# Optimization experiments

Hardware: AMD Instinct MI355X
Metric: run time of the kernel (lower is better)

## Reference

```python
import jax, jax.numpy as jnp
import numpy as np

B, N, D, O, H, R = 32, 1024, 1024, 1024, 512, 64
TOPK = 4
MAX_GAIN = 0.1
SCALE = 1.0
LN_EPS = 1e-5


def _dct_basis(dim, num_bases):
    pos = np.arange(dim, dtype=np.float64)[None, :]
    modes = np.arange(num_bases, dtype=np.float64)[:, None]
    basis = np.cos(np.pi / dim * (pos + 0.5) * modes)
    basis[0] = basis[0] / np.sqrt(2.0)
    basis = basis * np.sqrt(2.0 / dim)
    return jnp.asarray(basis, jnp.float32)


def setup_inputs() -> dict:
    key = jax.random.key(0)
    ks = jax.random.split(key, 16)
    s = 0.02
    return {
        'x': jax.random.normal(ks[0], (B, N, D), jnp.float32),
        'context': jax.random.normal(ks[1], (B, H), jnp.float32),
        'input_basis': _dct_basis(D, R),                       # [R, D] (buffer)
        'output_basis': s * jax.random.normal(ks[2], (R, O), jnp.float32),
        'ln_gamma': jnp.ones((D,), jnp.float32),
        'ln_beta': jnp.zeros((D,), jnp.float32),
        'w1': s * jax.random.normal(ks[3], (D, H), jnp.float32),
        'b1': jnp.zeros((H,), jnp.float32),
        'w2': s * jax.random.normal(ks[4], (H, H), jnp.float32),
        'b2': jnp.zeros((H,), jnp.float32),
        'wg': s * jax.random.normal(ks[5], (H, R * R), jnp.float32),
        'bg': jnp.zeros((R * R,), jnp.float32),
        'wl': s * jax.random.normal(ks[6], (H, R * R), jnp.float32),
        'bl': jnp.zeros((R * R,), jnp.float32),
        'wm': s * jax.random.normal(ks[7], (2 * H, R), jnp.float32),
        'bm': 1.5 * jnp.ones((R,), jnp.float32),
        'wgain': s * jax.random.normal(ks[8], (2 * H, R), jnp.float32),
        'bgain': jnp.zeros((R,), jnp.float32),
        'wgate': s * jax.random.normal(ks[9], (2 * H, 1), jnp.float32),
        'bgate': -1.0 * jnp.ones((1,), jnp.float32),
        'wa': s * jax.random.normal(ks[10], (2 * H, 1), jnp.float32),
        'ba': -1.0 * jnp.ones((1,), jnp.float32),
        'wb': s * jax.random.normal(ks[11], (2 * H, 1), jnp.float32),
        'bb': jnp.zeros((1,), jnp.float32),
    }


def _detail_summary(x, topk):
    # x: [B, N, D] with token 0 = CLS; pick topk highest-variance patch tokens
    pt = x[:, 1:]                                   # [B, N-1, D]
    pm = jnp.mean(pt, axis=1, keepdims=True)
    scores = jnp.mean((pt - pm) ** 2, axis=-1)      # [B, N-1]
    _, idx = jax.lax.top_k(scores, topk)            # [B, k]
    gathered = jnp.take_along_axis(pt, idx[:, :, None], axis=1)  # [B, k, D]
    return jnp.mean(gathered, axis=1)               # [B, D]


def _skew(a):
    return 0.5 * (a - jnp.swapaxes(a, -1, -2))


def reference(x, context, input_basis, output_basis, ln_gamma, ln_beta,
              w1, b1, w2, b2, wg, bg, wl, bl, wm, bm,
              wgain, bgain, wgate, bgate, wa, ba, wb, bb):
    b = x.shape[0]
    r = input_basis.shape[0]

    detail = _detail_summary(x, TOPK)               # [B, D]
    mu = jnp.mean(detail, axis=-1, keepdims=True)
    var = jnp.var(detail, axis=-1, keepdims=True)
    h = (detail - mu) * jax.lax.rsqrt(var + LN_EPS) * ln_gamma + ln_beta
    h = jax.nn.gelu(h @ w1 + b1, approximate=False)
    local_context = h @ w2 + b2                     # [B, H]
    fused = jnp.concatenate([context, local_context], axis=-1)  # [B, 2H]

    global_skew = _skew((context @ wg + bg).reshape(b, r, r))
    local_skew = _skew((local_context @ wl + bl).reshape(b, r, r))
    mode_mask = jax.nn.sigmoid(fused @ wm + bm)     # [B, R]
    # diag(m) @ A @ diag(m) == m_i * A_ij * m_j
    mg = mode_mask[:, :, None] * global_skew * mode_mask[:, None, :]
    ml = mode_mask[:, :, None] * local_skew * mode_mask[:, None, :]
    comm = ml @ mg - mg @ ml                        # [B, R, R]

    alpha = SCALE * 0.5 * jax.nn.sigmoid(fused @ wa + ba)   # [B, 1]
    beta = SCALE * 0.25 * jnp.tanh(fused @ wb + bb)         # [B, 1]
    omega = alpha[:, :, None] * 0.5 * (mg + ml) + beta[:, :, None] * (comm / 12.0)

    q = jax.vmap(jax.scipy.linalg.expm)(omega)              # [B, R, R]
    gains = 1.0 + MAX_GAIN * jnp.tanh(fused @ wgain + bgain)  # [B, R]
    operator = q * gains[:, None, :]                        # q @ diag(gains)

    proj = jnp.einsum('bnd,rd->bnr', x, input_basis)        # [B, N, R]
    gate = SCALE * jax.nn.sigmoid(fused @ wgate + bgate)    # [B, 1]
    transformed = jnp.einsum('bnr,brk->bnk', proj, operator)
    delta = gate[:, None, :] * (transformed - proj)         # [B, N, R]
    out = jnp.einsum('bnr,ro->bno', delta, output_basis)    # [B, N, O]
    return out
```

## Files before the change

### kernel.cpp

```cpp
#include <hip/hip_runtime.h>
#include <math.h>

#define NB 32
#define NN 1024
#define ND 1024
#define NO 1024
#define NH 512
#define NR 64

#define OFF_PM     0u
#define OFF_PMSQ   32768u
#define OFF_ROWSQ  32800u
#define OFF_G      65568u
#define OFF_H0     98336u
#define OFF_H1     131104u
#define OFF_LOCAL  147488u
#define OFF_P1     163872u
#define OFF_P2     294944u
#define OFF_PG     360480u
#define OFF_PL     884768u
#define OFF_MFIN   1675424u
#define OFF_C      1806496u
#define OFF_PROJ   3903648u
#define OFF_BT     6000800u

#define AK(av,k) ((k&3)==0?av[(k)>>2].x:((k&3)==1?av[(k)>>2].y:((k&3)==2?av[(k)>>2].z:av[(k)>>2].w)))

__global__ __launch_bounds__(256) void kT_basis(const float* __restrict__ basis, float* __restrict__ basisT){
  __shared__ float s[64][65];
  int d0 = blockIdx.x*64;
  int tid = threadIdx.x;
  #pragma unroll
  for(int i=0;i<16;i++){
    int idx = i*256 + tid;
    int r = idx>>6, dl = idx&63;
    s[r][dl] = basis[(size_t)r*ND + d0 + dl];
  }
  __syncthreads();
  #pragma unroll
  for(int i=0;i<16;i++){
    int idx = i*256 + tid;
    int dl = idx>>6, r = idx&63;
    basisT[(size_t)(d0+dl)*64 + r] = s[r][dl];
  }
}

__global__ __launch_bounds__(256) void k0_colsum(const float* __restrict__ x, float* __restrict__ part,
    float* __restrict__ rowsq){
  __shared__ float red[4][64];
  int tid = threadIdx.x;
  int nseg = blockIdx.x, b = blockIdx.y;
  int d4 = tid*4;
  int lane = tid & 63, wv = tid >> 6;
  const float* xp = x + (size_t)b*NN*ND + d4;
  int nstart = nseg*64; if(nseg==0) nstart = 1;
  int nend = nseg*64 + 64;
  float sx=0.f, sy=0.f, sz=0.f, sw=0.f;
  #pragma unroll 4
  for(int n=nstart; n<nend; n++){
    float4 v = *(const float4*)&xp[(size_t)n*ND];
    sx+=v.x; sy+=v.y; sz+=v.z; sw+=v.w;
    float s = v.x*v.x + v.y*v.y + v.z*v.z + v.w*v.w;
    #pragma unroll
    for(int o=32;o>0;o>>=1) s += __shfl_down(s, o);
    if(lane==0) red[wv][n - nseg*64] = s;
  }
  *(float4*)&part[(size_t)(b*16+nseg)*1024 + d4] = make_float4(sx,sy,sz,sw);
  __syncthreads();
  if(tid < 64 && !(nseg==0 && tid==0)){
    rowsq[b*1024 + nseg*64 + tid] = red[0][tid]+red[1][tid]+red[2][tid]+red[3][tid];
  }
}

__global__ __launch_bounds__(256) void k1_pmreduce(const float* __restrict__ part, float* __restrict__ pm, float* __restrict__ pmsq){
  __shared__ float red[256];
  int b = blockIdx.x, tid = threadIdx.x;
  float acc = 0.f;
  #pragma unroll
  for(int i=0;i<4;i++){
    int d = i*256 + tid;
    float s = 0.f;
    #pragma unroll
    for(int ks=0;ks<16;ks++) s += part[(size_t)(b*16+ks)*1024 + d];
    float p = s * (1.0f/1023.0f);
    pm[b*1024+d] = p;
    acc += p*p;
  }
  red[tid] = acc; __syncthreads();
  for(int o=128;o>0;o>>=1){ if(tid<o) red[tid]+=red[tid+o]; __syncthreads(); }
  if(tid==0) pmsq[b] = red[0]*(1.0f/1024.0f);
}

__global__ __launch_bounds__(256) void k2_proj(const float* __restrict__ x, const float* __restrict__ bT,
    const float* __restrict__ pm, float* __restrict__ proj, float* __restrict__ projp,
    float* __restrict__ G, float* __restrict__ Gp){
  __shared__ __align__(16) float xs[64][68];
  __shared__ __align__(16) float bs[64][68];
  int tid = threadIdx.x;
  int row0 = blockIdx.x*64;
  int b = row0 >> 10;
  int kh = blockIdx.y;
  int kbase = kh*512;
  int lrow = tid>>4, lkv = tid&15;
  int rg = tid>>4, cg = tid&15;
  float acc[4][4];
  #pragma unroll
  for(int i_=0;i_<4;i_++){ acc[i_][0]=0.f; acc[i_][1]=0.f; acc[i_][2]=0.f; acc[i_][3]=0.f; }
  float gp[4]={0.f,0.f,0.f,0.f};
  int sw = ((lkv>>1)&3)<<2;
  for(int kc=0;kc<8;kc++){
    int k0 = kbase + kc*64;
    float4 p4 = *(const float4*)&pm[(size_t)b*ND + k0 + lkv*4];
    #pragma unroll
    for(int i=0;i<4;i++){
      int r = lrow + 16*i;
      float4 v = *(const float4*)&x[((size_t)(row0+r))*ND + k0 + lkv*4];
      int rs = r ^ sw;
      xs[lkv*4+0][rs]=v.x; xs[lkv*4+1][rs]=v.y; xs[lkv*4+2][rs]=v.z; xs[lkv*4+3][rs]=v.w;
      gp[i] += v.x*p4.x + v.y*p4.y + v.z*p4.z + v.w*p4.w;
    }
    #pragma unroll
    for(int i=0;i<4;i++){
      int idx = tid + 256*i;
      int kk = idx>>4, kv = idx&15;
      *(float4*)&bs[kk][kv*4] = *(const float4*)&bT[((size_t)(k0+kk))*64 + kv*4];
    }
    __syncthreads();
    #pragma unroll 8
    for(int kk=0;kk<64;kk++){
      float4 a = *(const float4*)&xs[kk][ (rg ^ ((kk>>3)&3)) << 2 ];
      float4 bb= *(const float4*)&bs[kk][cg*4];
      float ar[4]={a.x,a.y,a.z,a.w};
      float br[4]={bb.x,bb.y,bb.z,bb.w};
      #pragma unroll
      for(int i_=0;i_<4;i_++){
        #pragma unroll
        for(int j_=0;j_<4;j_++) acc[i_][j_] += ar[i_]*br[j_];
      }
    }
    __syncthreads();
  }
  float* dst = kh ? projp : proj;
  #pragma unroll
  for(int i_=0;i_<4;i_++){
    float4 v = make_float4(acc[i_][0],acc[i_][1],acc[i_][2],acc[i_][3]);
    *(float4*)&dst[((size_t)(row0 + rg*4 + i_))*NR + cg*4] = v;
  }
  __syncthreads();
  #pragma unroll
  for(int i=0;i<4;i++){ int r = lrow+16*i; bs[r][lkv]=gp[i]; }
  __syncthreads();
  if(tid<64){
    float g=0.f;
    #pragma unroll
    for(int c=0;c<16;c++) g += bs[tid][c];
    if(kh) Gp[row0+tid] = g; else G[row0+tid] = g;
  }
}

__global__ __launch_bounds__(256) void k2_red(float* __restrict__ proj, const float* __restrict__ projp){
  int id = blockIdx.x*256 + threadIdx.x;
  float4 a = *(const float4*)&proj[(size_t)id*4];
  float4 p = *(const float4*)&projp[(size_t)id*4];
  a.x+=p.x; a.y+=p.y; a.z+=p.z; a.w+=p.w;
  *(float4*)&proj[(size_t)id*4] = a;
}

__global__ __launch_bounds__(256) void k3_detail(const float* __restrict__ x, const float* __restrict__ rowsq,
    const float* __restrict__ G, const float* __restrict__ Gp, const float* __restrict__ pmsq,
    const float* __restrict__ gamma_, const float* __restrict__ beta_, float* __restrict__ h0){
  __shared__ float sc[1024];
  __shared__ float rv[256];
  __shared__ int ri[256];
  __shared__ int topi[4];
  __shared__ float mred[256];
  int b = blockIdx.x, tid = threadIdx.x;
  float ps = pmsq[b];
  const float invD = 1.0f/1024.0f;
  for(int n=tid;n<1024;n+=256)
    sc[n] = (n==0) ? -INFINITY : (rowsq[b*1024+n] - 2.0f*(G[b*1024+n]+Gp[b*1024+n]))*invD + ps;
  __syncthreads();
  for(int t=0;t<4;t++){
    float bv = -INFINITY; int bi = 0x7fffffff;
    for(int n=tid;n<1024;n+=256){
      float v = sc[n];
      if(v>bv || (v==bv && n<bi)){ bv=v; bi=n; }
    }
    rv[tid]=bv; ri[tid]=bi;
    __syncthreads();
    for(int o=128;o>0;o>>=1){
      if(tid<o){
        float v=rv[tid+o]; int ii=ri[tid+o];
        if(v>rv[tid] || (v==rv[tid] && ii<ri[tid])){ rv[tid]=v; ri[tid]=ii; }
      }
      __syncthreads();
    }
    if(tid==0){ topi[t]=ri[0]; sc[ri[0]] = -INFINITY; }
    __syncthreads();
  }
  int i0=topi[0], i1=topi[1], i2=topi[2], i3=topi[3];
  float dv[4]; float dsum=0.f;
  #pragma unroll
  for(int jj=0;jj<4;jj++){
    int d = tid + jj*256;
    float v = 0.25f*(x[((size_t)(b*NN+i0))*ND+d] + x[((size_t)(b*NN+i1))*ND+d]
                   + x[((size_t)(b*NN+i2))*ND+d] + x[((size_t)(b*NN+i3))*ND+d]);
    dv[jj]=v; dsum+=v;
  }
  mred[tid]=dsum; __syncthreads();
  for(int o=128;o>0;o>>=1){ if(tid<o) mred[tid]+=mred[tid+o]; __syncthreads(); }
  float mu = mred[0]*invD;
  __syncthreads();
  float vs=0.f;
  #pragma unroll
  for(int jj=0;jj<4;jj++){ float t2=dv[jj]-mu; vs+=t2*t2; }
  mred[tid]=vs; __syncthreads();
  for(int o=128;o>0;o>>=1){ if(tid<o) mred[tid]+=mred[tid+o]; __syncthreads(); }
  float var = mred[0]*invD;
  float rstd = rsqrtf(var + 1e-5f);
  #pragma unroll
  for(int jj=0;jj<4;jj++){
    int d = tid + jj*256;
    h0[b*1024+d] = (dv[jj]-mu)*rstd*gamma_[d] + beta_[d];
  }
}

__global__ __launch_bounds__(256) void gemm32_partial(const float* __restrict__ V, const float* __restrict__ W,
      float* __restrict__ part, int Kd, int Ncols){
  __shared__ __align__(16) float Vs[128][36];
  int col = blockIdx.x*256 + threadIdx.x;
  int k0 = blockIdx.y*128;
  for(int i=threadIdx.x; i<4096; i+=256){ int r=i>>7, k=i&127; Vs[k][r] = V[(size_t)r*Kd + k0 + k]; }
  __syncthreads();
  float acc[32];
  #pragma unroll
  for(int r=0;r<32;r++) acc[r]=0.f;
  #pragma unroll 4
  for(int k=0;k<128;k++){
    float wv = W[(size_t)(k0+k)*Ncols + col];
    #pragma unroll
    for(int r4=0;r4<8;r4++){
      float4 v = *(const float4*)&Vs[k][r4*4];
      acc[r4*4+0]+=v.x*wv; acc[r4*4+1]+=v.y*wv; acc[r4*4+2]+=v.z*wv; acc[r4*4+3]+=v.w*wv;
    }
  }
  #pragma unroll
  for(int r=0;r<32;r++) part[((size_t)(blockIdx.y*32 + r))*Ncols + col] = acc[r];
}

__global__ __launch_bounds__(256) void gemm32_gl(const float* __restrict__ ctx, const float* __restrict__ lcl,
    const float* __restrict__ wg, const float* __restrict__ wl,
    float* __restrict__ pg, float* __restrict__ pl){
  __shared__ __align__(16) float Vs[128][36];
  const float* V = blockIdx.z ? lcl : ctx;
  const float* W = blockIdx.z ? wl : wg;
  float* part    = blockIdx.z ? pl : pg;
  int col = blockIdx.x*256 + threadIdx.x;
  int k0 = blockIdx.y*128;
  for(int i=threadIdx.x; i<4096; i+=256){ int r=i>>7, k=i&127; Vs[k][r] = V[(size_t)r*512 + k0 + k]; }
  __syncthreads();
  float acc[32];
  #pragma unroll
  for(int r=0;r<32;r++) acc[r]=0.f;
  #pragma unroll 4
  for(int k=0;k<128;k++){
    float wv = W[(size_t)(k0+k)*4096 + col];
    #pragma unroll
    for(int r4=0;r4<8;r4++){
      float4 v = *(const float4*)&Vs[k][r4*4];
      acc[r4*4+0]+=v.x*wv; acc[r4*4+1]+=v.y*wv; acc[r4*4+2]+=v.z*wv; acc[r4*4+3]+=v.w*wv;
    }
  }
  #pragma unroll
  for(int r=0;r<32;r++) part[((size_t)(blockIdx.y*32 + r))*4096 + col] = acc[r];
}

__global__ __launch_bounds__(256) void k_red_gelu(const float* __restrict__ part, const float* __restrict__ b1, float* __restrict__ h1){
  int id = blockIdx.x*256 + threadIdx.x;
  int b_ = id >> 9, j = id & 511;
  float s = b1[j];
  #pragma unroll
  for(int ks=0;ks<8;ks++) s += part[(size_t)(ks*32+b_)*512 + j];
  h1[id] = 0.5f*s*(1.0f + erff(s*0.70710678118654752440f));
}
__global__ __launch_bounds__(256) void k_red_local(const float* __restrict__ part, const float* __restrict__ b2, float* __restrict__ lcl){
  int id = blockIdx.x*256 + threadIdx.x;
  int b_ = id >> 9, j = id & 511;
  float s = b2[j];
  #pragma unroll
  for(int ks=0;ks<4;ks++) s += part[(size_t)(ks*32+b_)*512 + j];
  lcl[id] = s;
}

__global__ __launch_bounds__(1024) void k7_fused(
    const float* __restrict__ pg, const float* __restrict__ pl,
    const float* __restrict__ bg, const float* __restrict__ bl,
    const float* __restrict__ context, const float* __restrict__ lcl,
    const float* __restrict__ wm, const float* __restrict__ bm,
    const float* __restrict__ wgain, const float* __restrict__ bgain,
    const float* __restrict__ wgate, const float* __restrict__ bgate,
    const float* __restrict__ wa, const float* __restrict__ ba,
    const float* __restrict__ wb, const float* __restrict__ bb,
    float* __restrict__ Mfin){
  __shared__ __align__(16) float B0s[64][68];
  __shared__ __align__(16) float B1s[64][68];
  __shared__ __align__(16) float B2s[64][68];
  __shared__ float fs[1024];
  __shared__ float redm[16][64];
  __shared__ float redg[16][64];
  __shared__ float wra[16], wrb[16], wrg[16];
  __shared__ float msks[64], gainss[64];
  __shared__ float colsum[64];
  __shared__ float sABG[3];
  __shared__ int ssh;
  int b = blockIdx.x, tid = threadIdx.x;

  int ig = tid>>5, jg = tid&31;
  int i0 = ig*2, j0 = jg*2;
  #pragma unroll
  for(int di=0;di<2;di++){
    #pragma unroll
    for(int dj=0;dj<2;dj++){
      int i=i0+di, jx=j0+dj, c=i*64+jx;
      float sg = bg[c], sl = bl[c];
      #pragma unroll
      for(int ks=0;ks<4;ks++){
        sg += pg[(size_t)(ks*32+b)*4096 + c];
        sl += pl[(size_t)(ks*32+b)*4096 + c];
      }
      B0s[i][jx] = sg; B1s[i][jx] = sl;
    }
  }
  fs[tid] = (tid < 512) ? context[b*512 + tid] : lcl[b*512 + tid - 512];
  __syncthreads();
  int j = tid & 63, kq = tid >> 6;
  {
    const float* wmp = wm    + (size_t)(kq*64)*64 + j;
    const float* wgp = wgain + (size_t)(kq*64)*64 + j;
    float am = 0.f, ag = 0.f;
    #pragma unroll 8
    for(int k=0;k<64;k++){
      float f = fs[kq*64 + k];
      am += f * wmp[k*64];
      ag += f * wgp[k*64];
    }
    redm[kq][j] = am; redg[kq][j] = ag;
    float f = fs[tid];
    float pa = f*wa[tid], pb = f*wb[tid], pgt = f*wgate[tid];
    #pragma unroll
    for(int o=32;o>0;o>>=1){
      pa += __shfl_down(pa, o);
      pb += __shfl_down(pb, o);
      pgt += __shfl_down(pgt, o);
    }
    if(j == 0){ wra[kq]=pa; wrb[kq]=pb; wrg[kq]=pgt; }
  }
  __syncthreads();
  for(int o=8;o>0;o>>=1){
    if(kq < o){ redm[kq][j] += redm[kq+o][j]; redg[kq][j] += redg[kq+o][j]; }
    __syncthreads();
  }
  if(tid < 64){
    float m = redm[0][tid] + bm[tid];
    msks[tid] = 1.0f/(1.0f+expf(-m));
    float g = redg[0][tid] + bgain[tid];
    gainss[tid] = 1.0f + 0.1f*tanhf(g);
  }
  if(tid == 0){
    float sa=0.f, sb=0.f, sg2=0.f;
    #pragma unroll
    for(int i=0;i<16;i++){ sa+=wra[i]; sb+=wrb[i]; sg2+=wrg[i]; }
    sABG[0] = 0.5f/(1.0f+expf(-(sa+ba[0])));
    sABG[1] = 0.25f*tanhf(sb+bb[0]);
    sABG[2] = 1.0f/(1.0f+expf(-(sg2+bgate[0])));
  }
  __syncthreads();
  float alpha = sABG[0], bta = sABG[1], gate = sABG[2];
  float mgr[2][2], mlr[2][2];
  #pragma unroll
  for(int di=0;di<2;di++){
    #pragma unroll
    for(int dj=0;dj<2;dj++){
      int i=i0+di, jx=j0+dj;
      float mm_ = msks[i]*msks[jx]*0.5f;
      mgr[di][dj] = mm_*(B0s[i][jx]-B0s[jx][i]);
      mlr[di][dj] = mm_*(B1s[i][jx]-B1s[jx][i]);
    }
  }
  __syncthreads();
  #pragma unroll
  for(int di=0;di<2;di++){
    #pragma unroll
    for(int dj=0;dj<2;dj++){
      int i=i0+di, jx=j0+dj;
      B0s[i][jx] = mgr[di][dj];
      B1s[i][jx] = mlr[di][dj];
    }
  }
  __syncthreads();
  int ir = tid>>4, cgc = tid&15;
  int jc = cgc*4;
  float4 av[16];
  {
    const float* rowp = &B1s[ir][0];
    #pragma unroll
    for(int q=0;q<16;q++) av[q] = *(const float4*)(rowp + q*4);
    float4 t1 = make_float4(0.f,0.f,0.f,0.f);
    #pragma unroll
    for(int k=0;k<64;k++){
      float4 bv = *(const float4*)&B0s[k][jc];
      float a = AK(av,k);
      t1.x += a*bv.x; t1.y += a*bv.y; t1.z += a*bv.z; t1.w += a*bv.w;
    }
    const float* rowq = &B0s[ir][0];
    #pragma unroll
    for(int q=0;q<16;q++) av[q] = *(const float4*)(rowq + q*4);
    float4 t2 = make_float4(0.f,0.f,0.f,0.f);
    #pragma unroll
    for(int k=0;k<64;k++){
      float4 bv = *(const float4*)&B1s[k][jc];
      float a = AK(av,k);
      t2.x += a*bv.x; t2.y += a*bv.y; t2.z += a*bv.z; t2.w += a*bv.w;
    }
    float4 cm = make_float4(t1.x-t2.x, t1.y-t2.y, t1.z-t2.z, t1.w-t2.w);
    *(float4*)&B2s[ir][jc] = cm;
  }
  __syncthreads();
  {
    const float bc = bta*(1.0f/12.0f);
    float4 g4 = *(const float4*)&B0s[ir][jc];
    float4 l4 = *(const float4*)&B1s[ir][jc];
    float4 c4 = *(const float4*)&B2s[ir][jc];
    float4 o4;
    o4.x = alpha*0.5f*(g4.x+l4.x) + bc*c4.x;
    o4.y = alpha*0.5f*(g4.y+l4.y) + bc*c4.y;
    o4.z = alpha*0.5f*(g4.z+l4.z) + bc*c4.z;
    o4.w = alpha*0.5f*(g4.w+l4.w) + bc*c4.w;
    *(float4*)&B0s[ir][jc] = o4;
  }
  __syncthreads();
  if(tid<64){
    float s=0.f;
    for(int i=0;i<64;i++) s += fabsf(B0s[i][tid]);
    colsum[tid]=s;
  }
  __syncthreads();
  if(tid==0){
    float m=0.f;
    for(int jx=0;jx<64;jx++) m = fmaxf(m, colsum[jx]);
    int s=0;
    while(m>0.5f && s<30){ m*=0.5f; s++; }
    ssh = s;
  }
  __syncthreads();
  int sh = ssh;
  float scl = ldexpf(1.0f, -sh);
  {
    float4 a4 = *(const float4*)&B0s[ir][jc];
    a4.x*=scl; a4.y*=scl; a4.z*=scl; a4.w*=scl;
    *(float4*)&B0s[ir][jc] = a4;
    float4 p4;
    p4.x = ((ir==jc+0)?1.0f:0.0f) + a4.x*0.125f;
    p4.y = ((ir==jc+1)?1.0f:0.0f) + a4.y*0.125f;
    p4.z = ((ir==jc+2)?1.0f:0.0f) + a4.z*0.125f;
    p4.w = ((ir==jc+3)?1.0f:0.0f) + a4.w*0.125f;
    *(float4*)&B1s[ir][jc] = p4;
  }
  __syncthreads();
  {
    const float* rowp = &B0s[ir][0];
    #pragma unroll
    for(int q=0;q<16;q++) av[q] = *(const float4*)(rowp + q*4);
  }
  float* P = &B1s[0][0];
  float* T = &B2s[0][0];
  for(int kk=7;kk>=1;kk--){
    float4 acc = make_float4(0.f,0.f,0.f,0.f);
    #pragma unroll
    for(int k=0;k<64;k++){
      float4 bv = *(const float4*)&P[(size_t)k*68 + jc];
      float a = AK(av,k);
      acc.x += a*bv.x; acc.y += a*bv.y; acc.z += a*bv.z; acc.w += a*bv.w;
    }
    float inv = 1.0f/(float)kk;
    float4 o4;
    o4.x = ((ir==jc+0)?1.0f:0.0f) + acc.x*inv;
    o4.y = ((ir==jc+1)?1.0f:0.0f) + acc.y*inv;
    o4.z = ((ir==jc+2)?1.0f:0.0f) + acc.z*inv;
    o4.w = ((ir==jc+3)?1.0f:0.0f) + acc.w*inv;
    *(float4*)&T[(size_t)ir*68 + jc] = o4;
    __syncthreads();
    float* tmp = P; P = T; T = tmp;
  }
  float* S = (P == &B1s[0][0]) ? &B2s[0][0] : &B1s[0][0];
  for(int t=0;t<sh;t++){
    #pragma unroll
    for(int q=0;q<16;q++) av[q] = *(const float4*)(P + (size_t)ir*68 + q*4);
    float4 acc = make_float4(0.f,0.f,0.f,0.f);
    #pragma unroll
    for(int k=0;k<64;k++){
      float4 bv = *(const float4*)&P[(size_t)k*68 + jc];
      float a = AK(av,k);
      acc.x += a*bv.x; acc.y += a*bv.y; acc.z += a*bv.z; acc.w += a*bv.w;
    }
    *(float4*)&S[(size_t)ir*68 + jc] = acc;
    __syncthreads();
    float* tmp = P; P = S; S = tmp;
  }
  {
    float4 q4 = *(const float4*)&P[(size_t)ir*68 + jc];
    float4 v;
    v.x = gate*(q4.x*gainss[jc+0] - ((ir==jc+0)?1.0f:0.0f));
    v.y = gate*(q4.y*gainss[jc+1] - ((ir==jc+1)?1.0f:0.0f));
    v.z = gate*(q4.z*gainss[jc+2] - ((ir==jc+2)?1.0f:0.0f));
    v.w = gate*(q4.w*gainss[jc+3] - ((ir==jc+3)?1.0f:0.0f));
    *(float4*)&Mfin[(size_t)b*4096 + ir*64 + jc] = v;
  }
}

__global__ __launch_bounds__(256) void k8_cmat(const float* __restrict__ Mfin, const float* __restrict__ ob, float* __restrict__ C){
  __shared__ __align__(16) float MT[64][68];
  int b = blockIdx.y; int o0 = blockIdx.x*128;
  int tid = threadIdx.x;
  for(int idx=tid; idx<4096; idx+=256){ int i=idx>>6, k=idx&63; MT[k][i] = Mfin[b*4096+idx]; }
  __syncthreads();
  int cg = tid&31, rg = tid>>5;
  float acc[8][4];
  #pragma unroll
  for(int r=0;r<8;r++){ acc[r][0]=0.f; acc[r][1]=0.f; acc[r][2]=0.f; acc[r][3]=0.f; }
  for(int k=0;k<64;k++){
    float4 bv = *(const float4*)&ob[(size_t)k*NO + o0 + cg*4];
    float4 a0 = *(const float4*)&MT[k][rg*8];
    float4 a1 = *(const float4*)&MT[k][rg*8+4];
    float arr[8]={a0.x,a0.y,a0.z,a0.w,a1.x,a1.y,a1.z,a1.w};
    #pragma unroll
    for(int r=0;r<8;r++){
      acc[r][0]+=arr[r]*bv.x; acc[r][1]+=arr[r]*bv.y; acc[r][2]+=arr[r]*bv.z; acc[r][3]+=arr[r]*bv.w;
    }
  }
  #pragma unroll
  for(int r=0;r<8;r++){
    *(float4*)&C[((size_t)(b*64 + rg*8+r))*NO + o0 + cg*4] = make_float4(acc[r][0],acc[r][1],acc[r][2],acc[r][3]);
  }
}

__global__ __launch_bounds__(256) void k9_out(const float* __restrict__ proj, const float* __restrict__ C, float* __restrict__ out){
  __shared__ __align__(16) float PT[64][132];
  __shared__ __align__(16) float CS[64][68];
  int b = blockIdx.z; int row0 = blockIdx.y*128; int o0 = blockIdx.x*64;
  int tid = threadIdx.x;
  #pragma unroll
  for(int i=0;i<8;i++){
    int f = tid + 256*i; int r = f>>4; int kv = f&15;
    float4 v = *(const float4*)&proj[((size_t)(b*NN + row0 + r))*NR + kv*4];
    PT[kv*4+0][r]=v.x; PT[kv*4+1][r]=v.y; PT[kv*4+2][r]=v.z; PT[kv*4+3][r]=v.w;
  }
  #pragma unroll
  for(int i=0;i<4;i++){
    int f = tid + 256*i; int k = f>>4; int kv = f&15;
    *(float4*)&CS[k][kv*4] = *(const float4*)&C[((size_t)(b*NR + k))*NO + o0 + kv*4];
  }
  __syncthreads();
  int rg = tid>>4, cg = tid&15;
  float acc[8][4];
  #pragma unroll
  for(int r=0;r<8;r++){ acc[r][0]=0.f; acc[r][1]=0.f; acc[r][2]=0.f; acc[r][3]=0.f; }
  #pragma unroll 8
  for(int k=0;k<64;k++){
    float4 bv = *(const float4*)&CS[k][cg*4];
    float4 a0 = *(const float4*)&PT[k][rg*8];
    float4 a1 = *(const float4*)&PT[k][rg*8+4];
    float arr[8]={a0.x,a0.y,a0.z,a0.w,a1.x,a1.y,a1.z,a1.w};
    #pragma unroll
    for(int r=0;r<8;r++){
      acc[r][0]+=arr[r]*bv.x; acc[r][1]+=arr[r]*bv.y; acc[r][2]+=arr[r]*bv.z; acc[r][3]+=arr[r]*bv.w;
    }
  }
  #pragma unroll
  for(int r=0;r<8;r++){
    *(float4*)&out[((size_t)(b*NN + row0 + rg*8 + r))*NO + o0 + cg*4] =
        make_float4(acc[r][0],acc[r][1],acc[r][2],acc[r][3]);
  }
}

extern "C" void kernel_launch(void* const* d_in, const int* in_sizes, int n_in,
                              void* d_out, int out_size, void* d_ws, size_t ws_size,
                              hipStream_t stream) {
  (void)in_sizes; (void)n_in; (void)out_size; (void)ws_size;
  const float* x       = (const float*)d_in[0];
  const float* context = (const float*)d_in[1];
  const float* ibasis  = (const float*)d_in[2];
  const float* obasis  = (const float*)d_in[3];
  const float* lng     = (const float*)d_in[4];
  const float* lnb     = (const float*)d_in[5];
  const float* w1      = (const float*)d_in[6];
  const float* b1      = (const float*)d_in[7];
  const float* w2      = (const float*)d_in[8];
  const float* b2      = (const float*)d_in[9];
  const float* wg      = (const float*)d_in[10];
  const float* bg      = (const float*)d_in[11];
  const float* wl      = (const float*)d_in[12];
  const float* bl      = (const float*)d_in[13];
  const float* wm      = (const float*)d_in[14];
  const float* bm      = (const float*)d_in[15];
  const float* wgain   = (const float*)d_in[16];
  const float* bgain   = (const float*)d_in[17];
  const float* wgate   = (const float*)d_in[18];
  const float* bgate   = (const float*)d_in[19];
  const float* wa      = (const float*)d_in[20];
  const float* ba      = (const float*)d_in[21];
  const float* wb      = (const float*)d_in[22];
  const float* bb      = (const float*)d_in[23];
  float* out = (float*)d_out;
  float* ws  = (float*)d_ws;

  float* pm    = ws + OFF_PM;
  float* pmsq  = ws + OFF_PMSQ;
  float* rowsq = ws + OFF_ROWSQ;
  float* G     = ws + OFF_G;
  float* h0    = ws + OFF_H0;
  float* h1    = ws + OFF_H1;
  float* lcl   = ws + OFF_LOCAL;
  float* p1    = ws + OFF_P1;
  float* p2    = ws + OFF_P2;
  float* pg_   = ws + OFF_PG;
  float* part  = ws + OFF_PG;
  float* Gp    = ws + OFF_PG;
  float* pl_   = ws + OFF_PL;
  float* Mfin  = ws + OFF_MFIN;
  float* Cb    = ws + OFF_C;
  float* projp = ws + OFF_C;
  float* proj  = ws + OFF_PROJ;
  float* bT    = ws + OFF_BT;

  kT_basis<<<16,256,0,stream>>>(ibasis, bT);
  k0_colsum<<<dim3(16,NB),256,0,stream>>>(x, part, rowsq);
  k1_pmreduce<<<NB,256,0,stream>>>(part, pm, pmsq);
  k2_proj<<<dim3(512,2),256,0,stream>>>(x, bT, pm, proj, projp, G, Gp);
  k2_red<<<2048,256,0,stream>>>(proj, projp);
  k3_detail<<<NB,256,0,stream>>>(x, rowsq, G, Gp, pmsq, lng, lnb, h0);
  gemm32_partial<<<dim3(2,8),256,0,stream>>>(h0, w1, p1, 1024, 512);
  k_red_gelu<<<64,256,0,stream>>>(p1, b1, h1);
  gemm32_partial<<<dim3(2,4),256,0,stream>>>(h1, w2, p2, 512, 512);
  k_red_local<<<64,256,0,stream>>>(p2, b2, lcl);
  gemm32_gl<<<dim3(16,4,2),256,0,stream>>>(context, lcl, wg, wl, pg_, pl_);
  k7_fused<<<NB,1024,0,stream>>>(pg_, pl_, bg, bl, context, lcl, wm, bm, wgain, bgain,
                                 wgate, bgate, wa, ba, wb, bb, Mfin);
  k8_cmat<<<dim3(8,NB),256,0,stream>>>(Mfin, obasis, Cb);
  k9_out<<<dim3(16,8,NB),256,0,stream>>>(proj, Cb, out);
}
```

Baseline: 580.6 us.

## Fuse small reduction kernels into consumers and enlarge output GEMM tile with swizzle

Merges the basis transpose into the column-sum kernel as extra blocks. Folds the GELU and bias reductions of split-K partials into the loads of the following GEMMs and k7, which removes three small launches and their intermediate buffers. Widens the final output GEMM tile to 128x128 with 8x8 per-thread accumulators and XOR-swizzled shared memory to avoid bank conflicts. This raises per-thread reuse and register use. The reductions are now recomputed redundantly inside each consuming block.

```diff
diff --git a/kernel.cpp b/kernel.cpp
--- a/kernel.cpp
+++ b/kernel.cpp
@@ -13,8 +13,6 @@
 #define OFF_ROWSQ  32800u
 #define OFF_G      65568u
 #define OFF_H0     98336u
-#define OFF_H1     131104u
-#define OFF_LOCAL  147488u
 #define OFF_P1     163872u
 #define OFF_P2     294944u
 #define OFF_PG     360480u
@@ -26,29 +24,30 @@
 
 #define AK(av,k) ((k&3)==0?av[(k)>>2].x:((k&3)==1?av[(k)>>2].y:((k&3)==2?av[(k)>>2].z:av[(k)>>2].w)))
 
-__global__ __launch_bounds__(256) void kT_basis(const float* __restrict__ basis, float* __restrict__ basisT){
-  __shared__ float s[64][65];
-  int d0 = blockIdx.x*64;
+__global__ __launch_bounds__(256) void k0_colsum(const float* __restrict__ x, const float* __restrict__ basis,
+    float* __restrict__ part, float* __restrict__ rowsq, float* __restrict__ basisT){
   int tid = threadIdx.x;
-  #pragma unroll
-  for(int i=0;i<16;i++){
-    int idx = i*256 + tid;
-    int r = idx>>6, dl = idx&63;
-    s[r][dl] = basis[(size_t)r*ND + d0 + dl];
-  }
-  __syncthreads();
-  #pragma unroll
-  for(int i=0;i<16;i++){
-    int idx = i*256 + tid;
-    int dl = idx>>6, r = idx&63;
-    basisT[(size_t)(d0+dl)*64 + r] = s[r][dl];
-  }
-}
-
-__global__ __launch_bounds__(256) void k0_colsum(const float* __restrict__ x, float* __restrict__ part,
-    float* __restrict__ rowsq){
+  if(blockIdx.x == 16){
+    int yy = blockIdx.y;
+    if(yy >= 16) return;
+    __shared__ float s[64][65];
+    int d0 = yy*64;
+    #pragma unroll
+    for(int i=0;i<16;i++){
+      int idx = i*256 + tid;
+      int r = idx>>6, dl = idx&63;
+      s[r][dl] = basis[(size_t)r*ND + d0 + dl];
+    }
+    __syncthreads();
+    #pragma unroll
+    for(int i=0;i<16;i++){
+      int idx = i*256 + tid;
+      int dl = idx>>6, r = idx&63;
+      basisT[(size_t)(d0+dl)*64 + r] = s[r][dl];
+    }
+    return;
+  }
   __shared__ float red[4][64];
-  int tid = threadIdx.x;
   int nseg = blockIdx.x, b = blockIdx.y;
   int d4 = tid*4;
   int lane = tid & 63, wv = tid >> 6;
@@ -248,17 +247,56 @@
   for(int r=0;r<32;r++) part[((size_t)(blockIdx.y*32 + r))*Ncols + col] = acc[r];
 }
 
-__global__ __launch_bounds__(256) void gemm32_gl(const float* __restrict__ ctx, const float* __restrict__ lcl,
-    const float* __restrict__ wg, const float* __restrict__ wl,
+__global__ __launch_bounds__(256) void gemm32_h2(const float* __restrict__ p1, const float* __restrict__ b1,
+      const float* __restrict__ W, float* __restrict__ part){
+  __shared__ __align__(16) float Vs[128][36];
+  int col = blockIdx.x*256 + threadIdx.x;
+  int k0 = blockIdx.y*128;
+  for(int i=threadIdx.x; i<4096; i+=256){
+    int r=i>>7, k=i&127; int j = k0 + k;
+    float s = b1[j];
+    #pragma unroll
+    for(int ks=0;ks<8;ks++) s += p1[(size_t)(ks*32+r)*512 + j];
+    Vs[k][r] = 0.5f*s*(1.0f + erff(s*0.70710678118654752440f));
+  }
+  __syncthreads();
+  float acc[32];
+  #pragma unroll
+  for(int r=0;r<32;r++) acc[r]=0.f;
+  #pragma unroll 4
+  for(int k=0;k<128;k++){
+    float wv = W[(size_t)(k0+k)*512 + col];
+    #pragma unroll
+    for(int r4=0;r4<8;r4++){
+      float4 v = *(const float4*)&Vs[k][r4*4];
+      acc[r4*4+0]+=v.x*wv; acc[r4*4+1]+=v.y*wv; acc[r4*4+2]+=v.z*wv; acc[r4*4+3]+=v.w*wv;
+    }
+  }
+  #pragma unroll
+  for(int r=0;r<32;r++) part[((size_t)(blockIdx.y*32 + r))*512 + col] = acc[r];
+}
+
+__global__ __launch_bounds__(256) void gemm32_gl2(const float* __restrict__ ctx, const float* __restrict__ p2,
+    const float* __restrict__ b2, const float* __restrict__ wg, const float* __restrict__ wl,
     float* __restrict__ pg, float* __restrict__ pl){
   __shared__ __align__(16) float Vs[128][36];
-  const float* V = blockIdx.z ? lcl : ctx;
-  const float* W = blockIdx.z ? wl : wg;
-  float* part    = blockIdx.z ? pl : pg;
+  int z = blockIdx.z;
   int col = blockIdx.x*256 + threadIdx.x;
   int k0 = blockIdx.y*128;
-  for(int i=threadIdx.x; i<4096; i+=256){ int r=i>>7, k=i&127; Vs[k][r] = V[(size_t)r*512 + k0 + k]; }
-  __syncthreads();
+  if(z == 0){
+    for(int i=threadIdx.x; i<4096; i+=256){ int r=i>>7, k=i&127; Vs[k][r] = ctx[(size_t)r*512 + k0 + k]; }
+  } else {
+    for(int i=threadIdx.x; i<4096; i+=256){
+      int r=i>>7, k=i&127; int j = k0 + k;
+      float s = b2[j];
+      #pragma unroll
+      for(int ks=0;ks<4;ks++) s += p2[(size_t)(ks*32+r)*512 + j];
+      Vs[k][r] = s;
+    }
+  }
+  __syncthreads();
+  const float* W = z ? wl : wg;
+  float* part    = z ? pl : pg;
   float acc[32];
   #pragma unroll
   for(int r=0;r<32;r++) acc[r]=0.f;
@@ -275,27 +313,10 @@
   for(int r=0;r<32;r++) part[((size_t)(blockIdx.y*32 + r))*4096 + col] = acc[r];
 }
 
-__global__ __launch_bounds__(256) void k_red_gelu(const float* __restrict__ part, const float* __restrict__ b1, float* __restrict__ h1){
-  int id = blockIdx.x*256 + threadIdx.x;
-  int b_ = id >> 9, j = id & 511;
-  float s = b1[j];
-  #pragma unroll
-  for(int ks=0;ks<8;ks++) s += part[(size_t)(ks*32+b_)*512 + j];
-  h1[id] = 0.5f*s*(1.0f + erff(s*0.70710678118654752440f));
-}
-__global__ __launch_bounds__(256) void k_red_local(const float* __restrict__ part, const float* __restrict__ b2, float* __restrict__ lcl){
-  int id = blockIdx.x*256 + threadIdx.x;
-  int b_ = id >> 9, j = id & 511;
-  float s = b2[j];
-  #pragma unroll
-  for(int ks=0;ks<4;ks++) s += part[(size_t)(ks*32+b_)*512 + j];
-  lcl[id] = s;
-}
-
 __global__ __launch_bounds__(1024) void k7_fused(
     const float* __restrict__ pg, const float* __restrict__ pl,
     const float* __restrict__ bg, const float* __restrict__ bl,
-    const float* __restrict__ context, const float* __restrict__ lcl,
+    const float* __restrict__ context, const float* __restrict__ p2, const float* __restrict__ b2v,
     const float* __restrict__ wm, const float* __restrict__ bm,
     const float* __restrict__ wgain, const float* __restrict__ bgain,
     const float* __restrict__ wgate, const float* __restrict__ bgate,
@@ -331,7 +352,15 @@
       B0s[i][jx] = sg; B1s[i][jx] = sl;
     }
   }
-  fs[tid] = (tid < 512) ? context[b*512 + tid] : lcl[b*512 + tid - 512];
+  if(tid < 512){
+    fs[tid] = context[b*512 + tid];
+  } else {
+    int j2 = tid - 512;
+    float s = b2v[j2];
+    #pragma unroll
+    for(int ks=0;ks<4;ks++) s += p2[(size_t)(ks*32+b)*512 + j2];
+    fs[tid] = s;
+  }
   __syncthreads();
   int j = tid & 63, kq = tid >> 6;
   {
@@ -545,41 +574,65 @@
 }
 
 __global__ __launch_bounds__(256) void k9_out(const float* __restrict__ proj, const float* __restrict__ C, float* __restrict__ out){
-  __shared__ __align__(16) float PT[64][132];
-  __shared__ __align__(16) float CS[64][68];
-  int b = blockIdx.z; int row0 = blockIdx.y*128; int o0 = blockIdx.x*64;
+  __shared__ __align__(16) float PT[64*128];
+  __shared__ __align__(16) float CS[64*128];
+  int b = blockIdx.z; int row0 = blockIdx.y*128; int o0 = blockIdx.x*128;
   int tid = threadIdx.x;
   #pragma unroll
   for(int i=0;i<8;i++){
-    int f = tid + 256*i; int r = f>>4; int kv = f&15;
+    int f = tid + 256*i;
+    int r = f>>4; int kv = f&15;
     float4 v = *(const float4*)&proj[((size_t)(b*NN + row0 + r))*NR + kv*4];
-    PT[kv*4+0][r]=v.x; PT[kv*4+1][r]=v.y; PT[kv*4+2][r]=v.z; PT[kv*4+3][r]=v.w;
-  }
-  #pragma unroll
-  for(int i=0;i<4;i++){
-    int f = tid + 256*i; int k = f>>4; int kv = f&15;
-    *(float4*)&CS[k][kv*4] = *(const float4*)&C[((size_t)(b*NR + k))*NO + o0 + kv*4];
+    int sw = 4*(kv&7);
+    int rs = r ^ sw;
+    PT[(kv*4+0)*128 + rs] = v.x;
+    PT[(kv*4+1)*128 + rs] = v.y;
+    PT[(kv*4+2)*128 + rs] = v.z;
+    PT[(kv*4+3)*128 + rs] = v.w;
+  }
+  #pragma unroll
+  for(int i=0;i<8;i++){
+    int f = tid + 256*i;
+    int k = f>>5; int kv = f&31;
+    int col = kv*4;
+    int sc = (4*((k>>2)&7)) ^ (4*((col>>5)&1));
+    *(float4*)&CS[k*128 + (col ^ sc)] =
+        *(const float4*)&C[((size_t)(b*NR + k))*NO + o0 + col];
   }
   __syncthreads();
   int rg = tid>>4, cg = tid&15;
-  float acc[8][4];
-  #pragma unroll
-  for(int r=0;r<8;r++){ acc[r][0]=0.f; acc[r][1]=0.f; acc[r][2]=0.f; acc[r][3]=0.f; }
-  #pragma unroll 8
-  for(int k=0;k<64;k++){
-    float4 bv = *(const float4*)&CS[k][cg*4];
-    float4 a0 = *(const float4*)&PT[k][rg*8];
-    float4 a1 = *(const float4*)&PT[k][rg*8+4];
-    float arr[8]={a0.x,a0.y,a0.z,a0.w,a1.x,a1.y,a1.z,a1.w};
-    #pragma unroll
-    for(int r=0;r<8;r++){
-      acc[r][0]+=arr[r]*bv.x; acc[r][1]+=arr[r]*bv.y; acc[r][2]+=arr[r]*bv.z; acc[r][3]+=arr[r]*bv.w;
-    }
-  }
+  float acc[8][8];
   #pragma unroll
   for(int r=0;r<8;r++){
-    *(float4*)&out[((size_t)(b*NN + row0 + rg*8 + r))*NO + o0 + cg*4] =
-        make_float4(acc[r][0],acc[r][1],acc[r][2],acc[r][3]);
+    #pragma unroll
+    for(int c=0;c<8;c++) acc[r][c]=0.f;
+  }
+  int c0 = cg*8, c1 = cg*8+4;
+  int cbit = 4*((c0>>5)&1);
+  for(int kg=0; kg<16; kg++){
+    int swa = 4*(kg&7);
+    int base = kg*4*128;
+    int scb = swa ^ cbit;
+    #pragma unroll
+    for(int kk=0;kk<4;kk++){
+      float4 a0 = *(const float4*)&PT[base + kk*128 + ((rg*8)   ^ swa)];
+      float4 a1 = *(const float4*)&PT[base + kk*128 + ((rg*8+4) ^ swa)];
+      float4 b0 = *(const float4*)&CS[base + kk*128 + (c0 ^ scb)];
+      float4 b1 = *(const float4*)&CS[base + kk*128 + (c1 ^ scb)];
+      float ar[8]={a0.x,a0.y,a0.z,a0.w,a1.x,a1.y,a1.z,a1.w};
+      float br[8]={b0.x,b0.y,b0.z,b0.w,b1.x,b1.y,b1.z,b1.w};
+      #pragma unroll
+      for(int r=0;r<8;r++){
+        #pragma unroll
+        for(int c=0;c<8;c++) acc[r][c] += ar[r]*br[c];
+      }
+    }
+  }
+  #pragma unroll
+  for(int r=0;r<8;r++){
+    size_t rowoff = ((size_t)(b*NN + row0 + rg*8 + r))*NO + o0 + cg*8;
+    *(float4*)&out[rowoff]   = make_float4(acc[r][0],acc[r][1],acc[r][2],acc[r][3]);
+    *(float4*)&out[rowoff+4] = make_float4(acc[r][4],acc[r][5],acc[r][6],acc[r][7]);
   }
 }
 
@@ -619,8 +672,6 @@
   float* rowsq = ws + OFF_ROWSQ;
   float* G     = ws + OFF_G;
   float* h0    = ws + OFF_H0;
-  float* h1    = ws + OFF_H1;
-  float* lcl   = ws + OFF_LOCAL;
   float* p1    = ws + OFF_P1;
   float* p2    = ws + OFF_P2;
   float* pg_   = ws + OFF_PG;
@@ -633,19 +684,16 @@
   float* proj  = ws + OFF_PROJ;
   float* bT    = ws + OFF_BT;
 
-  kT_basis<<<16,256,0,stream>>>(ibasis, bT);
-  k0_colsum<<<dim3(16,NB),256,0,stream>>>(x, part, rowsq);
+  k0_colsum<<<dim3(17,NB),256,0,stream>>>(x, ibasis, part, rowsq, bT);
   k1_pmreduce<<<NB,256,0,stream>>>(part, pm, pmsq);
   k2_proj<<<dim3(512,2),256,0,stream>>>(x, bT, pm, proj, projp, G, Gp);
   k2_red<<<2048,256,0,stream>>>(proj, projp);
   k3_detail<<<NB,256,0,stream>>>(x, rowsq, G, Gp, pmsq, lng, lnb, h0);
   gemm32_partial<<<dim3(2,8),256,0,stream>>>(h0, w1, p1, 1024, 512);
-  k_red_gelu<<<64,256,0,stream>>>(p1, b1, h1);
-  gemm32_partial<<<dim3(2,4),256,0,stream>>>(h1, w2, p2, 512, 512);
-  k_red_local<<<64,256,0,stream>>>(p2, b2, lcl);
-  gemm32_gl<<<dim3(16,4,2),256,0,stream>>>(context, lcl, wg, wl, pg_, pl_);
-  k7_fused<<<NB,1024,0,stream>>>(pg_, pl_, bg, bl, context, lcl, wm, bm, wgain, bgain,
+  gemm32_h2<<<dim3(2,4),256,0,stream>>>(p1, b1, w2, p2);
+  gemm32_gl2<<<dim3(16,4,2),256,0,stream>>>(context, p2, b2, wg, wl, pg_, pl_);
+  k7_fused<<<NB,1024,0,stream>>>(pg_, pl_, bg, bl, context, p2, b2, wm, bm, wgain, bgain,
                                  wgate, bgate, wa, ba, wb, bb, Mfin);
   k8_cmat<<<dim3(8,NB),256,0,stream>>>(Mfin, obasis, Cb);
-  k9_out<<<dim3(16,8,NB),256,0,stream>>>(proj, Cb, out);
-}
+  k9_out<<<dim3(8,8,NB),256,0,stream>>>(proj, Cb, out);
+}
```

Result: no change. 575.7 us (-0.8%).
